# Kernel tuning notes

Hardware: AMD Instinct MI355X
Metric: run time of the kernel (lower is better)

## Reference

```python
import jax, jax.numpy as jnp
import numpy as np

N_ATOMS = 50000
N_PAIRS = 600000
F = 128          # number_of_per_atom_features
RBF = 16         # number_of_radial_basis_functions
N_INT_RES = 3    # interaction residual blocks
N_OUT_RES = 2    # output residual blocks
N_PROPS = 2      # atomic properties (hardcoded in PhysNetModule)


def setup_inputs() -> dict:
    key = jax.random.key(0)
    ks = jax.random.split(key, 24)
    s = 1.0 / np.sqrt(F)
    inp = {
        "atomic_embedding": jax.random.normal(ks[0], (N_ATOMS, F), jnp.float32),
        "f_ij": jax.random.uniform(ks[1], (N_PAIRS, RBF), jnp.float32),
        "pair_indices": jax.random.randint(ks[2], (2, N_PAIRS), 0, N_ATOMS, jnp.int64),
        # attention_mask: Dense(RBF -> F, bias=False); zero-init in source, randomized here
        "Wg": jax.random.normal(ks[3], (RBF, F), jnp.float32) * (1.0 / np.sqrt(RBF)),
        "Wi": jax.random.normal(ks[4], (F, F), jnp.float32) * s,
        "bi": jnp.zeros((F,), jnp.float32),
        "Wj": jax.random.normal(ks[5], (F, F), jnp.float32) * s,
        "bj": jnp.zeros((F,), jnp.float32),
        "Wv": jax.random.normal(ks[6], (F, F), jnp.float32) * s,
        "bv": jnp.zeros((F,), jnp.float32),
        "gate": jnp.ones((F,), jnp.float32),
        "int_res_W1": jax.random.normal(ks[7], (N_INT_RES, F, F), jnp.float32) * s,
        "int_res_b1": jnp.zeros((N_INT_RES, F), jnp.float32),
        "int_res_W2": jax.random.normal(ks[8], (N_INT_RES, F, F), jnp.float32) * s,
        "int_res_b2": jnp.zeros((N_INT_RES, F), jnp.float32),
        "out_res_W1": jax.random.normal(ks[9], (N_OUT_RES, F, F), jnp.float32) * s,
        "out_res_b1": jnp.zeros((N_OUT_RES, F), jnp.float32),
        "out_res_W2": jax.random.normal(ks[10], (N_OUT_RES, F, F), jnp.float32) * s,
        "out_res_b2": jnp.zeros((N_OUT_RES, F), jnp.float32),
        # output head: Dense(F -> 2), zero-init in source, randomized here
        "Wo": jax.random.normal(ks[11], (F, N_PROPS), jnp.float32) * s,
        "bo": jnp.zeros((N_PROPS,), jnp.float32),
    }
    return inp


def _residual(x, W1, b1, W2, b2):
    # PhysNetResidual: x + Dense(Dense(act(x), act), linear)
    h = jax.nn.softplus(x)
    h = jax.nn.softplus(h @ W1 + b1)
    return x + h @ W2 + b2


def reference(atomic_embedding, f_ij, pair_indices,
              Wg, Wi, bi, Wj, bj, Wv, bv, gate,
              int_res_W1, int_res_b1, int_res_W2, int_res_b2,
              out_res_W1, out_res_b1, out_res_W2, out_res_b2,
              Wo, bo):
    idx_i, idx_j = pair_indices[0], pair_indices[1]

    # --- interaction module ---
    e = jax.nn.softplus(atomic_embedding)            # [N, F]
    g = f_ij @ Wg                                    # [E, F] attention mask (no bias)
    u = jax.nn.softplus(e @ Wi + bi)                 # [N, F] interaction_i
    m_j = jax.nn.softplus(e[idx_j] @ Wj + bj) * g    # [E, F] gather + gate
    u = u.at[idx_i].add(m_j)                         # scatter_add to i-atoms
    for k in range(N_INT_RES):
        u = _residual(u, int_res_W1[k], int_res_b1[k], int_res_W2[k], int_res_b2[k])
    u = jax.nn.softplus(u)
    v = gate * e + (u @ Wv + bv)                     # updated embedding [N, F]

    # --- output module ---
    x = v
    for k in range(N_OUT_RES):
        x = _residual(x, out_res_W1[k], out_res_b1[k], out_res_W2[k], out_res_b2[k])
    prediction = x @ Wo + bo                         # [N, 2]
    return prediction, v
```

## Files before the change

kernel.cpp:

```cpp
#include <hip/hip_runtime.h>
#include <math.h>

#define F 128
#define RBF 16
#define NATOMS 50000
#define NPAIRS 600000
#define NBLK 196

typedef float f32x4 __attribute__((ext_vector_type(4)));
typedef short s16x8 __attribute__((ext_vector_type(8)));

__device__ __forceinline__ float sp(float x) {
    return fmaxf(x, 0.f) + __logf(1.f + __expf(-fabsf(x)));
}
__device__ __forceinline__ short f2bf(float x) {
    unsigned u = __float_as_uint(x);
    u += 0x7FFFu + ((u >> 16) & 1u);
    return (short)(u >> 16);
}
__device__ __forceinline__ float bf2f(unsigned short u) {
    return __uint_as_float(((unsigned)u) << 16);
}

__global__ __launch_bounds__(256) void prep_w_k(
    const float* __restrict__ Wi, const float* __restrict__ Wj, const float* __restrict__ Wv,
    const float* __restrict__ iW1, const float* __restrict__ iW2,
    const float* __restrict__ oW1, const float* __restrict__ oW2,
    short* __restrict__ wpack)
{
    int o = blockIdx.x * 256 + threadIdx.x;
    if (o >= 13 * 16384) return;
    int mat = o >> 14;
    int rem = o & 16383;
    int j = rem & 7;
    int lane = (rem >> 3) & 63;
    int nt = (rem >> 9) & 7;
    int kc = rem >> 12;
    int k = kc * 32 + ((lane >> 4) << 3) + j;
    int n = nt * 16 + (lane & 15);
    const float* src;
    if (mat == 0) src = Wi;
    else if (mat == 1) src = Wj;
    else if (mat == 2) src = Wv;
    else if (mat < 6) src = iW1 + (size_t)(mat - 3) * 16384;
    else if (mat < 9) src = iW2 + (size_t)(mat - 6) * 16384;
    else if (mat < 11) src = oW1 + (size_t)(mat - 9) * 16384;
    else src = oW2 + (size_t)(mat - 11) * 16384;
    wpack[o] = f2bf(src[(size_t)k * F + n]);
}

template <int PRE>
__device__ __forceinline__ s16x8 load_a_frag(const float* __restrict__ in,
                                             int row, int nrows, int kc, int cg)
{
    s16x8 a;
    if (row < nrows) {
        const float* p = in + (size_t)row * F + kc * 32 + cg * 8;
        float4 x0 = *(const float4*)p;
        float4 x1 = *(const float4*)(p + 4);
        if (PRE) {
            x0.x = sp(x0.x); x0.y = sp(x0.y); x0.z = sp(x0.z); x0.w = sp(x0.w);
            x1.x = sp(x1.x); x1.y = sp(x1.y); x1.z = sp(x1.z); x1.w = sp(x1.w);
        }
        a[0] = f2bf(x0.x); a[1] = f2bf(x0.y); a[2] = f2bf(x0.z); a[3] = f2bf(x0.w);
        a[4] = f2bf(x1.x); a[5] = f2bf(x1.y); a[6] = f2bf(x1.z); a[7] = f2bf(x1.w);
    } else {
#pragma unroll
        for (int i = 0; i < 8; ++i) a[i] = 0;
    }
    return a;
}

template <int PRE, int POST, int DUAL>
__global__ __launch_bounds__(256) void mgemm_k(
    const float* __restrict__ in, const short* __restrict__ wpA,
    const float* __restrict__ bA, float* __restrict__ outA,
    const short* __restrict__ wpB, const float* __restrict__ bB,
    unsigned short* __restrict__ outB, int nrows)
{
    const int lane = threadIdx.x & 63;
    const int wv = threadIdx.x >> 6;
    const int grp = wv >> 1, half = wv & 1;
    const int r0 = blockIdx.x * 32 + grp * 16;
    const int cl = lane & 15, cg = lane >> 4;
    const int ntb = half * 4;

    s16x8 afr[4];
#pragma unroll
    for (int kc = 0; kc < 4; ++kc) afr[kc] = load_a_frag<PRE>(in, r0 + cl, nrows, kc, cg);

    f32x4 accA[4], accB[4];
#pragma unroll
    for (int n = 0; n < 4; ++n) {
        accA[n] = (f32x4){0.f, 0.f, 0.f, 0.f};
        accB[n] = (f32x4){0.f, 0.f, 0.f, 0.f};
    }

#pragma unroll
    for (int kc = 0; kc < 4; ++kc) {
        const s16x8* bpA = (const s16x8*)wpA + (size_t)(kc * 8 + ntb) * 64 + lane;
#pragma unroll
        for (int n = 0; n < 4; ++n) {
            s16x8 b = bpA[n * 64];
            accA[n] = __builtin_amdgcn_mfma_f32_16x16x32_bf16(afr[kc], b, accA[n], 0, 0, 0);
        }
        if (DUAL) {
            const s16x8* bpB = (const s16x8*)wpB + (size_t)(kc * 8 + ntb) * 64 + lane;
#pragma unroll
            for (int n = 0; n < 4; ++n) {
                s16x8 b = bpB[n * 64];
                accB[n] = __builtin_amdgcn_mfma_f32_16x16x32_bf16(afr[kc], b, accB[n], 0, 0, 0);
            }
        }
    }

#pragma unroll
    for (int n = 0; n < 4; ++n) {
        const int col = (ntb + n) * 16 + cl;
        const float ba = bA[col];
        const float bb = DUAL ? bB[col] : 0.f;
#pragma unroll
        for (int q = 0; q < 4; ++q) {
            const int row = r0 + cg * 4 + q;
            if (row < nrows) {
                const size_t o = (size_t)row * F + col;
                float val = accA[n][q] + ba;
                if (POST == 1) val = sp(val);
                outA[o] = val;
                if (DUAL) outB[o] = (unsigned short)f2bf(sp(accB[n][q] + bb));
            }
        }
    }
}

__device__ __forceinline__ void gemm_half(const short* __restrict__ wp, int lane, int ntb,
                                          const s16x8 afr[4], f32x4 acc[4])
{
#pragma unroll
    for (int n = 0; n < 4; ++n) acc[n] = (f32x4){0.f, 0.f, 0.f, 0.f};
#pragma unroll
    for (int kc = 0; kc < 4; ++kc) {
        const s16x8* bp = (const s16x8*)wp + (size_t)(kc * 8 + ntb) * 64 + lane;
#pragma unroll
        for (int n = 0; n < 4; ++n) {
            s16x8 b = bp[n * 64];
            acc[n] = __builtin_amdgcn_mfma_f32_16x16x32_bf16(afr[kc], b, acc[n], 0, 0, 0);
        }
    }
}

template <int FIRST>
__device__ __forceinline__ void residual_half(
    const float* __restrict__ u, f32x4 xreg[4],
    unsigned short* __restrict__ S, unsigned short* __restrict__ H,
    const short* __restrict__ wp1, const float* __restrict__ b1,
    const short* __restrict__ wp2, const float* __restrict__ b2,
    int r0, int nrows, int lane, int cl, int cg, int ntb)
{
    s16x8 afr[4];
    if (FIRST) {
#pragma unroll
        for (int kc = 0; kc < 4; ++kc) afr[kc] = load_a_frag<1>(u, r0 + cl, nrows, kc, cg);
    } else {
#pragma unroll
        for (int kc = 0; kc < 4; ++kc)
            afr[kc] = *(const s16x8*)(S + cl * 144 + kc * 32 + cg * 8);
    }
    f32x4 acc[4];
    gemm_half(wp1, lane, ntb, afr, acc);
#pragma unroll
    for (int n = 0; n < 4; ++n) {
        const int col = (ntb + n) * 16 + cl;
        const float bb = b1[col];
#pragma unroll
        for (int q = 0; q < 4; ++q)
            H[(cg * 4 + q) * 144 + col] = (unsigned short)f2bf(sp(acc[n][q] + bb));
    }
    __syncthreads();
#pragma unroll
    for (int kc = 0; kc < 4; ++kc)
        afr[kc] = *(const s16x8*)(H + cl * 144 + kc * 32 + cg * 8);
    gemm_half(wp2, lane, ntb, afr, acc);
#pragma unroll
    for (int n = 0; n < 4; ++n) {
        const int col = (ntb + n) * 16 + cl;
        const float bb = b2[col];
#pragma unroll
        for (int q = 0; q < 4; ++q) {
            float xv = xreg[n][q] + acc[n][q] + bb;
            xreg[n][q] = xv;
            S[(cg * 4 + q) * 144 + col] = (unsigned short)f2bf(sp(xv));
        }
    }
    __syncthreads();
}

__global__ __launch_bounds__(256, 4) void fused_tail_k(
    const float* __restrict__ u, const float* __restrict__ emb,
    const float* __restrict__ gate,
    const short* __restrict__ wpI1, const float* __restrict__ ib1,
    const short* __restrict__ wpI2, const float* __restrict__ ib2,
    const short* __restrict__ wpWv, const float* __restrict__ bvv,
    const short* __restrict__ wpO1, const float* __restrict__ ob1,
    const short* __restrict__ wpO2, const float* __restrict__ ob2,
    const float* __restrict__ Wo, const float* __restrict__ bo,
    float* __restrict__ vout, float* __restrict__ pred, int nrows)
{
    __shared__ unsigned short Sb[2][16 * 144];
    __shared__ unsigned short Hb[2][16 * 144];
    const int lane = threadIdx.x & 63;
    const int wv = threadIdx.x >> 6;
    const int grp = wv >> 1, half = wv & 1;
    const int r0 = blockIdx.x * 32 + grp * 16;
    const int cl = lane & 15, cg = lane >> 4;
    const int ntb = half * 4;
    unsigned short* S = Sb[grp];
    unsigned short* H = Hb[grp];

    f32x4 xreg[4];
#pragma unroll
    for (int n = 0; n < 4; ++n) {
        const int col = (ntb + n) * 16 + cl;
#pragma unroll
        for (int q = 0; q < 4; ++q) {
            const int row = r0 + cg * 4 + q;
            xreg[n][q] = (row < nrows) ? u[(size_t)row * F + col] : 0.f;
        }
    }

    residual_half<1>(u, xreg, S, H, wpI1, ib1, wpI2, ib2,
                     r0, nrows, lane, cl, cg, ntb);
    for (int k = 1; k < 3; ++k)
        residual_half<0>(u, xreg, S, H,
                         wpI1 + (size_t)k * 16384, ib1 + (size_t)k * F,
                         wpI2 + (size_t)k * 16384, ib2 + (size_t)k * F,
                         r0, nrows, lane, cl, cg, ntb);

    {
        s16x8 afr[4];
#pragma unroll
        for (int kc = 0; kc < 4; ++kc)
            afr[kc] = *(const s16x8*)(S + cl * 144 + kc * 32 + cg * 8);
        f32x4 acc[4];
        gemm_half(wpWv, lane, ntb, afr, acc);
        __syncthreads();
#pragma unroll
        for (int n = 0; n < 4; ++n) {
            const int col = (ntb + n) * 16 + cl;
            const float bb = bvv[col];
            const float gt = gate[col];
#pragma unroll
            for (int q = 0; q < 4; ++q) {
                const int row = r0 + cg * 4 + q;
                float val = acc[n][q] + bb;
                if (row < nrows) {
                    const size_t o = (size_t)row * F + col;
                    val += gt * sp(emb[o]);
                    vout[o] = val;
                }
                xreg[n][q] = val;
                S[(cg * 4 + q) * 144 + col] = (unsigned short)f2bf(sp(val));
            }
        }
        __syncthreads();
    }

    for (int k = 0; k < 2; ++k)
        residual_half<0>(u, xreg, S, H,
                         wpO1 + (size_t)k * 16384, ob1 + (size_t)k * F,
                         wpO2 + (size_t)k * 16384, ob2 + (size_t)k * F,
                         r0, nrows, lane, cl, cg, ntb);

    {
        float2 wo[4];
#pragma unroll
        for (int n = 0; n < 4; ++n)
            wo[n] = *(const float2*)(Wo + (size_t)((ntb + n) * 16 + cl) * 2);
        float* sc = (float*)S;
#pragma unroll
        for (int q = 0; q < 4; ++q) {
            float a0 = xreg[0][q] * wo[0].x + xreg[1][q] * wo[1].x
                     + xreg[2][q] * wo[2].x + xreg[3][q] * wo[3].x;
            float a1 = xreg[0][q] * wo[0].y + xreg[1][q] * wo[1].y
                     + xreg[2][q] * wo[2].y + xreg[3][q] * wo[3].y;
#pragma unroll
            for (int m = 1; m < 16; m <<= 1) {
                a0 += __shfl_xor(a0, m);
                a1 += __shfl_xor(a1, m);
            }
            if (cl == 0) {
                sc[half * 32 + (cg * 4 + q) * 2 + 0] = a0;
                sc[half * 32 + (cg * 4 + q) * 2 + 1] = a1;
            }
        }
        __syncthreads();
        if (half == 0 && lane < 16) {
            const int row = r0 + lane;
            if (row < nrows) {
                pred[(size_t)row * 2 + 0] = sc[lane * 2 + 0] + sc[32 + lane * 2 + 0] + bo[0];
                pred[(size_t)row * 2 + 1] = sc[lane * 2 + 1] + sc[32 + lane * 2 + 1] + bo[1];
            }
        }
    }
}

__global__ void zero_k(int* __restrict__ p, int n)
{
    int i = blockIdx.x * blockDim.x + threadIdx.x;
    if (i < n) p[i] = 0;
}

__global__ void hist_k(const int* __restrict__ idx_i, int* __restrict__ counts)
{
    int p = blockIdx.x * blockDim.x + threadIdx.x;
    if (p < NPAIRS) atomicAdd(&counts[idx_i[p]], 1);
}

__global__ __launch_bounds__(256) void scan1_k(
    const int* __restrict__ counts, int* __restrict__ bsum)
{
    __shared__ int red[256];
    const int t = threadIdx.x;
    const int i = blockIdx.x * 256 + t;
    red[t] = (i < NATOMS) ? counts[i] : 0;
    __syncthreads();
#pragma unroll
    for (int s = 128; s > 0; s >>= 1) {
        if (t < s) red[t] += red[t + s];
        __syncthreads();
    }
    if (t == 0) bsum[blockIdx.x] = red[0];
}

__global__ __launch_bounds__(256) void scan2_k(
    const int* __restrict__ bsum, int* __restrict__ bbase, int* __restrict__ offsets)
{
    __shared__ int sh[256];
    const int t = threadIdx.x;
    const int v = (t < NBLK) ? bsum[t] : 0;
    sh[t] = v;
    __syncthreads();
#pragma unroll
    for (int s = 1; s < 256; s <<= 1) {
        int add = (t >= s) ? sh[t - s] : 0;
        __syncthreads();
        sh[t] += add;
        __syncthreads();
    }
    if (t < NBLK) bbase[t] = sh[t] - v;
    if (t == 0) offsets[NATOMS] = NPAIRS;
}

__global__ __launch_bounds__(256) void scan3_k(
    const int* __restrict__ counts, const int* __restrict__ bbase,
    int* __restrict__ offsets, int* __restrict__ cursor)
{
    __shared__ int sh[256];
    const int t = threadIdx.x;
    const int i = blockIdx.x * 256 + t;
    const int v = (i < NATOMS) ? counts[i] : 0;
    sh[t] = v;
    __syncthreads();
#pragma unroll
    for (int s = 1; s < 256; s <<= 1) {
        int add = (t >= s) ? sh[t - s] : 0;
        __syncthreads();
        sh[t] += add;
        __syncthreads();
    }
    if (i < NATOMS) {
        const int off = bbase[blockIdx.x] + sh[t] - v;
        offsets[i] = off;
        cursor[i] = off;
    }
}

__global__ void scatter_k(const int* __restrict__ idx_i, const int* __restrict__ idx_j,
                          int* __restrict__ cursor, int* __restrict__ plist,
                          int* __restrict__ jlist)
{
    int p = blockIdx.x * blockDim.x + threadIdx.x;
    if (p < NPAIRS) {
        int pos = atomicAdd(&cursor[idx_i[p]], 1);
        plist[pos] = p;
        jlist[pos] = idx_j[p];
    }
}

__device__ __forceinline__ void gpair(const float* __restrict__ fp,
                                      const float* wg0, const float* wg1,
                                      float& g0, float& g1)
{
    float4 A = ((const float4*)fp)[0], B = ((const float4*)fp)[1];
    float4 C = ((const float4*)fp)[2], D = ((const float4*)fp)[3];
    g0 = A.x*wg0[0] + A.y*wg0[1] + A.z*wg0[2] + A.w*wg0[3]
       + B.x*wg0[4] + B.y*wg0[5] + B.z*wg0[6] + B.w*wg0[7]
       + C.x*wg0[8] + C.y*wg0[9] + C.z*wg0[10] + C.w*wg0[11]
       + D.x*wg0[12] + D.y*wg0[13] + D.z*wg0[14] + D.w*wg0[15];
    g1 = A.x*wg1[0] + A.y*wg1[1] + A.z*wg1[2] + A.w*wg1[3]
       + B.x*wg1[4] + B.y*wg1[5] + B.z*wg1[6] + B.w*wg1[7]
       + C.x*wg1[8] + C.y*wg1[9] + C.z*wg1[10] + C.w*wg1[11]
       + D.x*wg1[12] + D.y*wg1[13] + D.z*wg1[14] + D.w*wg1[15];
}

__global__ __launch_bounds__(256) void gather_k(
    const unsigned short* __restrict__ mj, const float* __restrict__ fij,
    const int* __restrict__ jlist, const int* __restrict__ plist,
    const int* __restrict__ offsets, const float* __restrict__ Wg,
    float* __restrict__ u)
{
    const int lane = threadIdx.x & 63;
    const int atom = blockIdx.x * 4 + (threadIdx.x >> 6);
    const int f0 = lane * 2;

    float wg0[16], wg1[16];
#pragma unroll
    for (int r = 0; r < 16; ++r) {
        float2 w = *(const float2*)(Wg + r * F + f0);
        wg0[r] = w.x; wg1[r] = w.y;
    }

    const int k0 = offsets[atom], k1 = offsets[atom + 1];
    float acc0 = 0.f, acc1 = 0.f;

    for (int k = k0; k < k1; k += 8) {
        int jv[8], pv[8];
#pragma unroll
        for (int t = 0; t < 8; ++t) {
            const int kk = (k + t < k1) ? (k + t) : (k1 - 1);
            jv[t] = jlist[kk];
            pv[t] = plist[kk];
        }
        unsigned m[8];
        const float* fp[8];
#pragma unroll
        for (int t = 0; t < 8; ++t) {
            const int js = __builtin_amdgcn_readfirstlane(jv[t]);
            const int ps = __builtin_amdgcn_readfirstlane(pv[t]);
            m[t] = *(const unsigned*)(mj + (size_t)js * F + f0);
            fp[t] = fij + (size_t)ps * RBF;
        }
#pragma unroll
        for (int t = 0; t < 8; ++t) {
            float g0, g1;
            gpair(fp[t], wg0, wg1, g0, g1);
            if (k + t >= k1) { g0 = 0.f; g1 = 0.f; }
            acc0 += bf2f((unsigned short)(m[t] & 0xFFFF)) * g0;
            acc1 += bf2f((unsigned short)(m[t] >> 16))    * g1;
        }
    }

    float2* up = (float2*)(u + (size_t)atom * F + f0);
    float2 old = *up;
    old.x += acc0; old.y += acc1;
    *up = old;
}

extern "C" void kernel_launch(void* const* d_in, const int* in_sizes, int n_in,
                              void* d_out, int out_size, void* d_ws, size_t ws_size,
                              hipStream_t stream)
{
    const float* emb   = (const float*)d_in[0];
    const float* fij   = (const float*)d_in[1];
    const int*   pidx  = (const int*)d_in[2];
    const float* Wg    = (const float*)d_in[3];
    const float* Wi    = (const float*)d_in[4];
    const float* bi    = (const float*)d_in[5];
    const float* Wj    = (const float*)d_in[6];
    const float* bj    = (const float*)d_in[7];
    const float* Wv    = (const float*)d_in[8];
    const float* bv    = (const float*)d_in[9];
    const float* gate  = (const float*)d_in[10];
    const float* iW1   = (const float*)d_in[11];
    const float* ib1   = (const float*)d_in[12];
    const float* iW2   = (const float*)d_in[13];
    const float* ib2   = (const float*)d_in[14];
    const float* oW1   = (const float*)d_in[15];
    const float* ob1   = (const float*)d_in[16];
    const float* oW2   = (const float*)d_in[17];
    const float* ob2   = (const float*)d_in[18];
    const float* Wo    = (const float*)d_in[19];
    const float* bo    = (const float*)d_in[20];

    const int* idx_i = pidx;
    const int* idx_j = pidx + NPAIRS;

    float* outp = (float*)d_out;
    float* pred = outp;
    float* v    = outp + (size_t)NATOMS * 2;

    const size_t NF = (size_t)NATOMS * F;
    float* u = (float*)d_ws;
    unsigned short* mj = (unsigned short*)(u + NF);
    short* wpack = (short*)(mj + NF);
    int* counts   = (int*)(wpack + 13 * 16384);
    int* offsets  = counts + NATOMS;
    int* cursor   = offsets + NATOMS + 1;
    int* plist    = cursor + NATOMS;
    int* jlist    = plist + NPAIRS;
    int* bsum     = jlist + NPAIRS;
    int* bbase    = bsum + NBLK;

    const short* wpWi = wpack;
    const short* wpWj = wpack + 1 * 16384;
    const short* wpWv = wpack + 2 * 16384;
    const short* wpI1 = wpack + 3 * 16384;
    const short* wpI2 = wpack + 6 * 16384;
    const short* wpO1 = wpack + 9 * 16384;
    const short* wpO2 = wpack + 11 * 16384;

    prep_w_k<<<(13 * 16384 + 255) / 256, 256, 0, stream>>>(Wi, Wj, Wv, iW1, iW2, oW1, oW2, wpack);
    zero_k<<<(NATOMS + 255) / 256, 256, 0, stream>>>(counts, NATOMS);
    hist_k<<<(NPAIRS + 255) / 256, 256, 0, stream>>>(idx_i, counts);
    scan1_k<<<NBLK, 256, 0, stream>>>(counts, bsum);
    scan2_k<<<1, 256, 0, stream>>>(bsum, bbase, offsets);
    scan3_k<<<NBLK, 256, 0, stream>>>(counts, bbase, offsets, cursor);
    scatter_k<<<(NPAIRS + 255) / 256, 256, 0, stream>>>(idx_i, idx_j, cursor, plist, jlist);

    mgemm_k<1, 1, 1><<<(NATOMS + 31) / 32, 256, 0, stream>>>(
        emb, wpWi, bi, u, wpWj, bj, mj, NATOMS);

    gather_k<<<(NATOMS + 3) / 4, 256, 0, stream>>>(
        mj, fij, jlist, plist, offsets, Wg, u);

    fused_tail_k<<<(NATOMS + 31) / 32, 256, 0, stream>>>(
        u, emb, gate,
        wpI1, ib1, wpI2, ib2,
        wpWv, bv,
        wpO1, ob1, wpO2, ob2,
        Wo, bo, v, pred, NATOMS);
}
```

Before: 267.6 us.

## Use hardware bf16 pack conversion, XOR-swizzle LDS tiles, memset counts

Replaces the software round-to-nearest float-to-bf16 conversion with the v_cvt_pk_bf16_f32 instruction, packing two values per conversion when building A fragments. The shared-memory S/H staging buffers get an XOR swizzle on the column index to reduce LDS bank conflicts. The custom zero kernel is swapped for hipMemsetAsync. Together these aim to cut ALU work and LDS conflict stalls in the fused tail kernel. The swizzle has to keep 8-element fragment reads contiguous, and the inline asm ties the code to gfx950.

```diff
diff --git a/kernel.cpp b/kernel.cpp
--- a/kernel.cpp
+++ b/kernel.cpp
@@ -13,6 +13,14 @@
 __device__ __forceinline__ float sp(float x) {
     return fmaxf(x, 0.f) + __logf(1.f + __expf(-fabsf(x)));
 }
+__device__ __forceinline__ unsigned cvtpk(float lo, float hi) {
+    unsigned r;
+    asm("v_cvt_pk_bf16_f32 %0, %1, %2" : "=v"(r) : "v"(lo), "v"(hi));
+    return r;
+}
+__device__ __forceinline__ unsigned short cvt1(float x) {
+    return (unsigned short)cvtpk(x, x);
+}
 __device__ __forceinline__ short f2bf(float x) {
     unsigned u = __float_as_uint(x);
     u += 0x7FFFu + ((u >> 16) & 1u);
@@ -20,6 +28,9 @@
 }
 __device__ __forceinline__ float bf2f(unsigned short u) {
     return __uint_as_float(((unsigned)u) << 16);
+}
+__device__ __forceinline__ int lds_idx(int row, int col) {
+    return (row * 144 + col) ^ ((row & 7) << 3);
 }
 
 __global__ __launch_bounds__(256) void prep_w_k(
@@ -53,7 +64,7 @@
 __device__ __forceinline__ s16x8 load_a_frag(const float* __restrict__ in,
                                              int row, int nrows, int kc, int cg)
 {
-    s16x8 a;
+    union { unsigned u[4]; s16x8 v; } pk;
     if (row < nrows) {
         const float* p = in + (size_t)row * F + kc * 32 + cg * 8;
         float4 x0 = *(const float4*)p;
@@ -62,13 +73,14 @@
             x0.x = sp(x0.x); x0.y = sp(x0.y); x0.z = sp(x0.z); x0.w = sp(x0.w);
             x1.x = sp(x1.x); x1.y = sp(x1.y); x1.z = sp(x1.z); x1.w = sp(x1.w);
         }
-        a[0] = f2bf(x0.x); a[1] = f2bf(x0.y); a[2] = f2bf(x0.z); a[3] = f2bf(x0.w);
-        a[4] = f2bf(x1.x); a[5] = f2bf(x1.y); a[6] = f2bf(x1.z); a[7] = f2bf(x1.w);
+        pk.u[0] = cvtpk(x0.x, x0.y);
+        pk.u[1] = cvtpk(x0.z, x0.w);
+        pk.u[2] = cvtpk(x1.x, x1.y);
+        pk.u[3] = cvtpk(x1.z, x1.w);
     } else {
-#pragma unroll
-        for (int i = 0; i < 8; ++i) a[i] = 0;
-    }
-    return a;
+        pk.u[0] = pk.u[1] = pk.u[2] = pk.u[3] = 0;
+    }
+    return pk.v;
 }
 
 template <int PRE, int POST, int DUAL>
@@ -127,7 +139,7 @@
                 float val = accA[n][q] + ba;
                 if (POST == 1) val = sp(val);
                 outA[o] = val;
-                if (DUAL) outB[o] = (unsigned short)f2bf(sp(accB[n][q] + bb));
+                if (DUAL) outB[o] = cvt1(sp(accB[n][q] + bb));
             }
         }
     }
@@ -164,7 +176,7 @@
     } else {
 #pragma unroll
         for (int kc = 0; kc < 4; ++kc)
-            afr[kc] = *(const s16x8*)(S + cl * 144 + kc * 32 + cg * 8);
+            afr[kc] = *(const s16x8*)(S + lds_idx(cl, kc * 32 + cg * 8));
     }
     f32x4 acc[4];
     gemm_half(wp1, lane, ntb, afr, acc);
@@ -174,12 +186,12 @@
         const float bb = b1[col];
 #pragma unroll
         for (int q = 0; q < 4; ++q)
-            H[(cg * 4 + q) * 144 + col] = (unsigned short)f2bf(sp(acc[n][q] + bb));
+            H[lds_idx(cg * 4 + q, col)] = cvt1(sp(acc[n][q] + bb));
     }
     __syncthreads();
 #pragma unroll
     for (int kc = 0; kc < 4; ++kc)
-        afr[kc] = *(const s16x8*)(H + cl * 144 + kc * 32 + cg * 8);
+        afr[kc] = *(const s16x8*)(H + lds_idx(cl, kc * 32 + cg * 8));
     gemm_half(wp2, lane, ntb, afr, acc);
 #pragma unroll
     for (int n = 0; n < 4; ++n) {
@@ -189,7 +201,7 @@
         for (int q = 0; q < 4; ++q) {
             float xv = xreg[n][q] + acc[n][q] + bb;
             xreg[n][q] = xv;
-            S[(cg * 4 + q) * 144 + col] = (unsigned short)f2bf(sp(xv));
+            S[lds_idx(cg * 4 + q, col)] = cvt1(sp(xv));
         }
     }
     __syncthreads();
@@ -240,7 +252,7 @@
         s16x8 afr[4];
 #pragma unroll
         for (int kc = 0; kc < 4; ++kc)
-            afr[kc] = *(const s16x8*)(S + cl * 144 + kc * 32 + cg * 8);
+            afr[kc] = *(const s16x8*)(S + lds_idx(cl, kc * 32 + cg * 8));
         f32x4 acc[4];
         gemm_half(wpWv, lane, ntb, afr, acc);
         __syncthreads();
@@ -259,7 +271,7 @@
                     vout[o] = val;
                 }
                 xreg[n][q] = val;
-                S[(cg * 4 + q) * 144 + col] = (unsigned short)f2bf(sp(val));
+                S[lds_idx(cg * 4 + q, col)] = cvt1(sp(val));
             }
         }
         __syncthreads();
@@ -302,12 +314,6 @@
             }
         }
     }
-}
-
-__global__ void zero_k(int* __restrict__ p, int n)
-{
-    int i = blockIdx.x * blockDim.x + threadIdx.x;
-    if (i < n) p[i] = 0;
 }
 
 __global__ void hist_k(const int* __restrict__ idx_i, int* __restrict__ counts)
@@ -510,7 +516,7 @@
     const short* wpO2 = wpack + 11 * 16384;
 
     prep_w_k<<<(13 * 16384 + 255) / 256, 256, 0, stream>>>(Wi, Wj, Wv, iW1, iW2, oW1, oW2, wpack);
-    zero_k<<<(NATOMS + 255) / 256, 256, 0, stream>>>(counts, NATOMS);
+    hipMemsetAsync(counts, 0, NATOMS * sizeof(int), stream);
     hist_k<<<(NPAIRS + 255) / 256, 256, 0, stream>>>(idx_i, counts);
     scan1_k<<<NBLK, 256, 0, stream>>>(counts, bsum);
     scan2_k<<<1, 256, 0, stream>>>(bsum, bbase, offsets);
```

After: 276.8 us. +3.5%, slower.

## Pack pair lists, widen gather batch, shrink tail blocks, memset counts

Applied to the files above, without the earlier changes.

Merges the separate j-index and pair-index lists into one int2 array, so gather_k issues one load per pair instead of two, and raises the gather batch from 8 to 16 pairs to keep more loads in flight. fused_tail_k now runs 128-thread blocks covering 16 rows with 6 blocks requested per CU. This shortens the time waves spend waiting at __syncthreads and changes occupancy. The zero kernel is replaced by hipMemsetAsync, and the f2bf return type is cleaned up. The larger gather batch raises register pressure.

```diff
diff --git a/kernel.cpp b/kernel.cpp
--- a/kernel.cpp
+++ b/kernel.cpp
@@ -13,10 +13,10 @@
 __device__ __forceinline__ float sp(float x) {
     return fmaxf(x, 0.f) + __logf(1.f + __expf(-fabsf(x)));
 }
-__device__ __forceinline__ short f2bf(float x) {
+__device__ __forceinline__ unsigned short f2bf(float x) {
     unsigned u = __float_as_uint(x);
     u += 0x7FFFu + ((u >> 16) & 1u);
-    return (short)(u >> 16);
+    return (unsigned short)(u >> 16);
 }
 __device__ __forceinline__ float bf2f(unsigned short u) {
     return __uint_as_float(((unsigned)u) << 16);
@@ -46,7 +46,7 @@
     else if (mat < 9) src = iW2 + (size_t)(mat - 6) * 16384;
     else if (mat < 11) src = oW1 + (size_t)(mat - 9) * 16384;
     else src = oW2 + (size_t)(mat - 11) * 16384;
-    wpack[o] = f2bf(src[(size_t)k * F + n]);
+    wpack[o] = (short)f2bf(src[(size_t)k * F + n]);
 }
 
 template <int PRE>
@@ -127,7 +127,7 @@
                 float val = accA[n][q] + ba;
                 if (POST == 1) val = sp(val);
                 outA[o] = val;
-                if (DUAL) outB[o] = (unsigned short)f2bf(sp(accB[n][q] + bb));
+                if (DUAL) outB[o] = f2bf(sp(accB[n][q] + bb));
             }
         }
     }
@@ -174,7 +174,7 @@
         const float bb = b1[col];
 #pragma unroll
         for (int q = 0; q < 4; ++q)
-            H[(cg * 4 + q) * 144 + col] = (unsigned short)f2bf(sp(acc[n][q] + bb));
+            H[(cg * 4 + q) * 144 + col] = f2bf(sp(acc[n][q] + bb));
     }
     __syncthreads();
 #pragma unroll
@@ -189,13 +189,13 @@
         for (int q = 0; q < 4; ++q) {
             float xv = xreg[n][q] + acc[n][q] + bb;
             xreg[n][q] = xv;
-            S[(cg * 4 + q) * 144 + col] = (unsigned short)f2bf(sp(xv));
+            S[(cg * 4 + q) * 144 + col] = f2bf(sp(xv));
         }
     }
     __syncthreads();
 }
 
-__global__ __launch_bounds__(256, 4) void fused_tail_k(
+__global__ __launch_bounds__(128, 6) void fused_tail_k(
     const float* __restrict__ u, const float* __restrict__ emb,
     const float* __restrict__ gate,
     const short* __restrict__ wpI1, const float* __restrict__ ib1,
@@ -206,16 +206,13 @@
     const float* __restrict__ Wo, const float* __restrict__ bo,
     float* __restrict__ vout, float* __restrict__ pred, int nrows)
 {
-    __shared__ unsigned short Sb[2][16 * 144];
-    __shared__ unsigned short Hb[2][16 * 144];
+    __shared__ unsigned short S[16 * 144];
+    __shared__ unsigned short H[16 * 144];
     const int lane = threadIdx.x & 63;
-    const int wv = threadIdx.x >> 6;
-    const int grp = wv >> 1, half = wv & 1;
-    const int r0 = blockIdx.x * 32 + grp * 16;
+    const int half = threadIdx.x >> 6;
+    const int r0 = blockIdx.x * 16;
     const int cl = lane & 15, cg = lane >> 4;
     const int ntb = half * 4;
-    unsigned short* S = Sb[grp];
-    unsigned short* H = Hb[grp];
 
     f32x4 xreg[4];
 #pragma unroll
@@ -259,7 +256,7 @@
                     vout[o] = val;
                 }
                 xreg[n][q] = val;
-                S[(cg * 4 + q) * 144 + col] = (unsigned short)f2bf(sp(val));
+                S[(cg * 4 + q) * 144 + col] = f2bf(sp(val));
             }
         }
         __syncthreads();
@@ -304,12 +301,6 @@
     }
 }
 
-__global__ void zero_k(int* __restrict__ p, int n)
-{
-    int i = blockIdx.x * blockDim.x + threadIdx.x;
-    if (i < n) p[i] = 0;
-}
-
 __global__ void hist_k(const int* __restrict__ idx_i, int* __restrict__ counts)
 {
     int p = blockIdx.x * blockDim.x + threadIdx.x;
@@ -376,14 +367,12 @@
 }
 
 __global__ void scatter_k(const int* __restrict__ idx_i, const int* __restrict__ idx_j,
-                          int* __restrict__ cursor, int* __restrict__ plist,
-                          int* __restrict__ jlist)
+                          int* __restrict__ cursor, int2* __restrict__ jplist)
 {
     int p = blockIdx.x * blockDim.x + threadIdx.x;
     if (p < NPAIRS) {
         int pos = atomicAdd(&cursor[idx_i[p]], 1);
-        plist[pos] = p;
-        jlist[pos] = idx_j[p];
+        jplist[pos] = make_int2(idx_j[p], p);
     }
 }
 
@@ -405,9 +394,8 @@
 
 __global__ __launch_bounds__(256) void gather_k(
     const unsigned short* __restrict__ mj, const float* __restrict__ fij,
-    const int* __restrict__ jlist, const int* __restrict__ plist,
-    const int* __restrict__ offsets, const float* __restrict__ Wg,
-    float* __restrict__ u)
+    const int2* __restrict__ jplist, const int* __restrict__ offsets,
+    const float* __restrict__ Wg, float* __restrict__ u)
 {
     const int lane = threadIdx.x & 63;
     const int atom = blockIdx.x * 4 + (threadIdx.x >> 6);
@@ -423,25 +411,24 @@
     const int k0 = offsets[atom], k1 = offsets[atom + 1];
     float acc0 = 0.f, acc1 = 0.f;
 
-    for (int k = k0; k < k1; k += 8) {
-        int jv[8], pv[8];
-#pragma unroll
-        for (int t = 0; t < 8; ++t) {
+    for (int k = k0; k < k1; k += 16) {
+        int2 jp[16];
+#pragma unroll
+        for (int t = 0; t < 16; ++t) {
             const int kk = (k + t < k1) ? (k + t) : (k1 - 1);
-            jv[t] = jlist[kk];
-            pv[t] = plist[kk];
-        }
-        unsigned m[8];
-        const float* fp[8];
-#pragma unroll
-        for (int t = 0; t < 8; ++t) {
-            const int js = __builtin_amdgcn_readfirstlane(jv[t]);
-            const int ps = __builtin_amdgcn_readfirstlane(pv[t]);
+            jp[t] = jplist[kk];
+        }
+        unsigned m[16];
+        const float* fp[16];
+#pragma unroll
+        for (int t = 0; t < 16; ++t) {
+            const int js = __builtin_amdgcn_readfirstlane(jp[t].x);
+            const int ps = __builtin_amdgcn_readfirstlane(jp[t].y);
             m[t] = *(const unsigned*)(mj + (size_t)js * F + f0);
             fp[t] = fij + (size_t)ps * RBF;
         }
 #pragma unroll
-        for (int t = 0; t < 8; ++t) {
+        for (int t = 0; t < 16; ++t) {
             float g0, g1;
             gpair(fp[t], wg0, wg1, g0, g1);
             if (k + t >= k1) { g0 = 0.f; g1 = 0.f; }
@@ -496,9 +483,8 @@
     int* counts   = (int*)(wpack + 13 * 16384);
     int* offsets  = counts + NATOMS;
     int* cursor   = offsets + NATOMS + 1;
-    int* plist    = cursor + NATOMS;
-    int* jlist    = plist + NPAIRS;
-    int* bsum     = jlist + NPAIRS;
+    int2* jplist  = (int2*)(cursor + NATOMS);
+    int* bsum     = (int*)(jplist + NPAIRS);
     int* bbase    = bsum + NBLK;
 
     const short* wpWi = wpack;
@@ -510,20 +496,20 @@
     const short* wpO2 = wpack + 11 * 16384;
 
     prep_w_k<<<(13 * 16384 + 255) / 256, 256, 0, stream>>>(Wi, Wj, Wv, iW1, iW2, oW1, oW2, wpack);
-    zero_k<<<(NATOMS + 255) / 256, 256, 0, stream>>>(counts, NATOMS);
+    hipMemsetAsync(counts, 0, NATOMS * sizeof(int), stream);
     hist_k<<<(NPAIRS + 255) / 256, 256, 0, stream>>>(idx_i, counts);
     scan1_k<<<NBLK, 256, 0, stream>>>(counts, bsum);
     scan2_k<<<1, 256, 0, stream>>>(bsum, bbase, offsets);
     scan3_k<<<NBLK, 256, 0, stream>>>(counts, bbase, offsets, cursor);
-    scatter_k<<<(NPAIRS + 255) / 256, 256, 0, stream>>>(idx_i, idx_j, cursor, plist, jlist);
+    scatter_k<<<(NPAIRS + 255) / 256, 256, 0, stream>>>(idx_i, idx_j, cursor, jplist);
 
     mgemm_k<1, 1, 1><<<(NATOMS + 31) / 32, 256, 0, stream>>>(
         emb, wpWi, bi, u, wpWj, bj, mj, NATOMS);
 
     gather_k<<<(NATOMS + 3) / 4, 256, 0, stream>>>(
-        mj, fij, jlist, plist, offsets, Wg, u);
-
-    fused_tail_k<<<(NATOMS + 31) / 32, 256, 0, stream>>>(
+        mj, fij, jplist, offsets, Wg, u);
+
+    fused_tail_k<<<(NATOMS + 15) / 16, 128, 0, stream>>>(
         u, emb, gate,
         wpI1, ib1, wpI2, ib2,
         wpWv, bv,
```

New measurement: 289.9 us. 8.3% more time.
